# Kernel tuning notes

Hardware: AMD Instinct MI355X
Metric: run time of the kernel (lower is better)

## Reference

```python
import jax, jax.numpy as jnp
import numpy as np
from jax import lax

# dims (see shape_source)
B, T = 256, 32
DQ, K, S, CTX = 128, 8, 4, 16
D = 2 * DQ + 1            # state_flat = [q (DQ), p (DQ), extra (1)]
EVO, DT, DAMP, TAU = 8, 0.2, 0.1, 1.0
TOPK = 2
GAMMA = 10.0              # gamma_pred
EPS = 1e-8


def _router(q, ctx, Wq, Wc, b):
    # chart routing: softmax over K charts, temperature TAU
    return jax.nn.softmax((q @ Wq + ctx @ Wc + b) / TAU, axis=-1)


def _decode_topk(x, w, rw, rb):
    # x: [B,D], w: [B,K] chart weights -> [B,S] logits via top-k chart mixture
    logits_k = jnp.einsum('bd,kvd->bkv', x, rw) + rb          # [B,K,S]
    wv, idx = lax.top_k(w, TOPK)
    wn = wv / jnp.clip(wv.sum(-1, keepdims=True), EPS)
    wm = jnp.zeros_like(w).at[jnp.arange(w.shape[0])[:, None], idx].set(wn)
    return jnp.einsum('bkv,bk->bv', logits_k, wm)


def setup_inputs() -> dict:
    key = jax.random.key(0)
    ks = jax.random.split(key, 11)
    return {
        'inputs': jax.random.randint(ks[0], (B, T), 0, 2),
        'targets': jax.random.randint(ks[1], (B, T), 0, S),
        'task_ids': jax.random.randint(ks[2], (B, T), 0, 2),
        'initial_state_flat': jax.random.normal(ks[3], (B, D), jnp.float32),
        'bit_embed': jax.random.normal(ks[4], (2, DQ), jnp.float32),
        'task_u_embed': jax.random.normal(ks[5], (2, DQ), jnp.float32),
        'router_ctx_embed': jax.random.normal(ks[6], (2, CTX), jnp.float32),
        'readout_weight': 0.1 * jax.random.normal(ks[7], (K, S, D), jnp.float32),
        'readout_bias': jnp.zeros((K, S), jnp.float32),
        'router_Wq': 0.1 * jax.random.normal(ks[8], (DQ, K), jnp.float32),
        'router_Wc': 0.1 * jax.random.normal(ks[9], (CTX, K), jnp.float32),
        'router_b': jnp.zeros((K,), jnp.float32),
        'A': 0.02 * jax.random.normal(ks[10], (K, DQ, DQ), jnp.float32),
    }


def reference(inputs, targets, task_ids, initial_state_flat, bit_embed, task_u_embed,
              router_ctx_embed, readout_weight, readout_bias, router_Wq, router_Wc,
              router_b, A):
    Bn, Tn = inputs.shape
    rows = jnp.arange(Bn)
    targets_prev = jnp.concatenate([jnp.zeros_like(targets[:, :1]), targets[:, :-1]], axis=1)

    def step(carry, xs):
        state, tF, tacc, tce, usage, tsum, tcnt, scw, scnt = carry
        bit_t, target_t, prev_t, task_t = xs
        u = jnp.tanh(bit_embed[bit_t]) + jnp.tanh(task_u_embed[task_t])   # [B,DQ]
        ctx = jnp.tanh(router_ctx_embed[task_t])                          # [B,CTX]

        def evo(st, _):
            q, p, s = st[:, :DQ], st[:, DQ:2 * DQ], st[:, 2 * DQ:]
            w = _router(q, ctx, router_Wq, router_Wc, router_b)           # [B,K]
            # chart-weighted mixture-of-experts dynamics (semi-implicit, damped)
            force = jnp.einsum('bk,kij,bj->bi', w, A, jnp.tanh(q))
            p_new = (1.0 - DT * DAMP) * p + DT * (force + u)
            q_new = q + DT * jnp.tanh(p_new)
            return jnp.concatenate([q_new, p_new, s], axis=1), w

        state, ws = lax.scan(evo, state, None, length=EVO)
        chart_w = ws[-1]                                                  # router w from last evo step
        q = state[:, :DQ]
        chart_w_next = _router(q, ctx, router_Wq, router_Wc, router_b)
        logits = _decode_topk(state, chart_w_next, readout_weight, readout_bias)  # [B,S]
        logits2 = logits[:, :2]
        tgt2 = jnp.where(task_t == 0, target_t, 0)
        ce2 = -jax.nn.log_softmax(logits2, axis=-1)[rows, tgt2]
        ce4 = -jax.nn.log_softmax(logits, axis=-1)[rows, target_t]
        mask2 = (task_t == 0).astype(jnp.float32)
        pred_error = mask2 * ce2 + (1.0 - mask2) * ce4
        chart_state_loss = -jnp.log(jnp.clip(chart_w, EPS))[rows, prev_t]
        F_t = GAMMA * (pred_error + chart_state_loss)

        pred = jnp.where(task_t == 0, jnp.argmax(logits2, -1), jnp.argmax(logits, -1))
        correct = (pred == target_t).astype(jnp.float32)
        task_oh = jax.nn.one_hot(task_t, 2, dtype=jnp.float32)
        mask4 = (task_t == 1).astype(jnp.float32)[:, None]
        state_oh = jax.nn.one_hot(prev_t, S, dtype=jnp.float32)
        carry = (state,
                 tF + F_t.mean(),
                 tacc + correct.mean(),
                 tce + pred_error.mean(),
                 usage + chart_w.sum(0),
                 tsum + (correct[:, None] * task_oh).sum(0),
                 tcnt + task_oh.sum(0),
                 scw + (state_oh * mask4).T @ chart_w,
                 scnt + (state_oh * mask4).sum(0))
        return carry, None

    zf = jnp.zeros((), jnp.float32)
    init = (initial_state_flat, zf, zf, zf,
            jnp.zeros((K,), jnp.float32), jnp.zeros((2,), jnp.float32),
            jnp.zeros((2,), jnp.float32), jnp.zeros((S, K), jnp.float32),
            jnp.zeros((S,), jnp.float32))
    xs = (inputs.T, targets.T, targets_prev.T, task_ids.T)
    (state, tF, tacc, tce, usage, tsum, tcnt, scw, scnt), _ = lax.scan(step, init, xs)

    mean_F = tF / Tn
    mean_acc = tacc / Tn
    mean_ce = tce / Tn
    per_task_acc = tsum / (tcnt + EPS)
    dist = usage / (usage.sum() + EPS)
    chart_ent = -(dist * jnp.log(dist + EPS)).sum()
    joint = scw / (scw.sum() + EPS)
    p_s = joint.sum(1, keepdims=True)
    p_c = joint.sum(0, keepdims=True)
    mi = (joint * (jnp.log(joint + EPS) - jnp.log(p_s + EPS) - jnp.log(p_c + EPS))).sum()
    mi = jnp.where(scw.sum() > 0, jnp.clip(mi, 0.0), 0.0)
    return (mean_F, mean_acc, mean_ce, usage, chart_ent, per_task_acc, scw, scnt, mi)
```

## Files before the change

kernel.cpp:

```cpp
#include <hip/hip_runtime.h>
#include <hip/hip_fp16.h>

namespace {
constexpr int kT = 32, kDQ = 128, kK = 8, kS = 4, kCTX = 16, kD = 257, kEVO = 8;
constexpr float kDT = 0.2f, kDAMP = 0.1f, kGAMMA = 10.0f, kEPS = 1e-8f;

typedef _Float16 half8 __attribute__((ext_vector_type(8)));
typedef float f32x4 __attribute__((ext_vector_type(4)));
typedef unsigned u32x4 __attribute__((ext_vector_type(4)));

__device__ __forceinline__ unsigned packh2(float lo, float hi) {
  __half l = __float2half(lo), h = __float2half(hi);
  return (unsigned)__half_as_ushort(l) | ((unsigned)__half_as_ushort(h) << 16);
}
__device__ __forceinline__ float fast_tanh(float x) {
  float e = __expf(2.f * x);
  return 1.f - 2.f / (e + 1.f);
}
}

extern "C" __global__ void __launch_bounds__(512, 2)
seq_main(const int* __restrict__ inputs, const int* __restrict__ targets,
         const int* __restrict__ task_ids, const float* __restrict__ st0,
         const float* __restrict__ bit_emb, const float* __restrict__ task_u,
         const float* __restrict__ ctx_emb, const float* __restrict__ rw_g,
         const float* __restrict__ rb_g, const float* __restrict__ Wq_g,
         const float* __restrict__ Wc_g, const float* __restrict__ b_g,
         const float* __restrict__ A_g, float* __restrict__ ws) {
  const int tid = threadIdx.x, b = blockIdx.x;
  const int lane = tid & 63, w = tid >> 6;
  const int g = lane >> 4, c = lane & 15;
  const int g2 = lane >> 3, j = lane & 7;
  const int i_own = 16 * w + c;

  __shared__ __align__(16) float rw_l[kK * kS * kD];
  __shared__ __align__(16) float u4_l[4][kDQ];
  __shared__ __align__(16) float q_l[2][kDQ];
  __shared__ __align__(16) float p_l[kDQ];
  __shared__ __align__(16) unsigned tq_l[2][64];
  __shared__ __align__(16) float wq_ctx2[2][kK];
  __shared__ float chartw_l[kK];
  __shared__ float cwnext_l[kK];
  __shared__ float rb_l[kK * kS];
  __shared__ float lk_l[kK * kS];
  __shared__ float acc_l[64];
  __shared__ float s_l;

  for (int idx = tid; idx < kK * kS * kD; idx += 512) rw_l[idx] = rw_g[idx];
  if (tid < kK * kS) rb_l[tid] = rb_g[tid];
  if (tid == 0) s_l = st0[b * kD + 2 * kDQ];
  if (tid < 64) acc_l[tid] = 0.f;
  {
    int cb = tid >> 7, i = tid & 127;
    u4_l[cb][i] = tanhf(bit_emb[(cb & 1) * kDQ + i]) + tanhf(task_u[(cb >> 1) * kDQ + i]);
  }
  if (tid < 16) {
    int tk = tid >> 3, kk = tid & 7;
    float s = b_g[kk];
    #pragma unroll
    for (int cc = 0; cc < kCTX; cc++) s += tanhf(ctx_emb[tk * kCTX + cc]) * Wc_g[cc * kK + kk];
    wq_ctx2[tk][kk] = s;
  }

  const int kA = (c & 3) + 4 * ((c >> 3) & 1);
  const int ipar = (c >> 2) & 1;
  u32x4 afr[8][4];
  #pragma unroll
  for (int mt = 0; mt < 8; mt++) {
    const float* arow = A_g + ((size_t)kA * kDQ + (16 * w + 2 * mt + ipar)) * kDQ;
    #pragma unroll
    for (int ks = 0; ks < 4; ks++) {
      const float4* p4 = reinterpret_cast<const float4*>(arow + 32 * ks + 8 * g);
      float4 f0 = p4[0], f1 = p4[1];
      u32x4 v;
      v.x = packh2(f0.x, f0.y); v.y = packh2(f0.z, f0.w);
      v.z = packh2(f1.x, f1.y); v.w = packh2(f1.z, f1.w);
      afr[mt][ks] = v;
    }
  }
  float wqr[16];
  #pragma unroll
  for (int m = 0; m < 16; m++) wqr[m] = Wq_g[(16 * j + m) * kK + g2];

  float q = st0[b * kD + i_own];
  float p = st0[b * kD + kDQ + i_own];
  if (g == 0) {
    q_l[0][i_own] = q;
    float tv = fast_tanh(q);
    float to = __shfl_xor(tv, 1);
    if (!(c & 1)) tq_l[0][i_own >> 1] = packh2(tv, to);
  }
  __syncthreads();

  const float ctx0k = wq_ctx2[0][g2], ctx1k = wq_ctx2[1][g2];
  const int srl0 = 32 * (lane >> 5) + j;
  const int boff = b * kT;

  auto rdot = [&](const float* qb) -> float {
    const float4* q4 = reinterpret_cast<const float4*>(qb + 16 * j);
    float4 a0 = q4[0], a1 = q4[1], a2 = q4[2], a3 = q4[3];
    float part = a0.x * wqr[0] + a0.y * wqr[1] + a0.z * wqr[2] + a0.w * wqr[3]
               + a1.x * wqr[4] + a1.y * wqr[5] + a1.z * wqr[6] + a1.w * wqr[7]
               + a2.x * wqr[8] + a2.y * wqr[9] + a2.z * wqr[10] + a2.w * wqr[11]
               + a3.x * wqr[12] + a3.y * wqr[13] + a3.z * wqr[14] + a3.w * wqr[15];
    part += __shfl_xor(part, 1); part += __shfl_xor(part, 2); part += __shfl_xor(part, 4);
    return part;
  };
  auto rsmax = [&](float wlog, float ctxk) -> float {
    float lg = wlog + ctxk;
    float mx = lg;
    mx = fmaxf(mx, __shfl_xor(mx, 8));
    mx = fmaxf(mx, __shfl_xor(mx, 16));
    mx = fmaxf(mx, __shfl_xor(mx, 32));
    float ex = __expf(lg - mx);
    float sm = ex;
    sm += __shfl_xor(sm, 8); sm += __shfl_xor(sm, 16); sm += __shfl_xor(sm, 32);
    return ex / sm;
  };

  float ws0, ws1, ws2, ws3;
  {
    const int task0 = task_ids[boff];
    float wlog = rdot(q_l[0]);
    float wv = rsmax(wlog, task0 ? ctx1k : ctx0k);
    ws0 = __shfl(wv, srl0);      ws1 = __shfl(wv, srl0 + 8);
    ws2 = __shfl(wv, srl0 + 16); ws3 = __shfl(wv, srl0 + 24);
  }

  int sb = 0;
  for (int t = 0; t < kT; t++) {
    const int bit = inputs[boff + t];
    const int task = task_ids[boff + t];
    const int tasknx = (t < kT - 1) ? task_ids[boff + t + 1] : 0;
    const float u_own = u4_l[task * 2 + bit][i_own];

    for (int e = 0; e < kEVO; e++) {
      const u32x4* tq4 = reinterpret_cast<const u32x4*>(tq_l[sb]);
      f32x4 ac[8];
      #pragma unroll
      for (int mt = 0; mt < 8; mt++) ac[mt] = f32x4{0.f, 0.f, 0.f, 0.f};
      #pragma unroll
      for (int ks = 0; ks < 4; ks++) {
        half8 bf = __builtin_bit_cast(half8, tq4[4 * ks + g]);
        #pragma unroll
        for (int mt = 0; mt < 8; mt++)
          ac[mt] = __builtin_amdgcn_mfma_f32_16x16x32_f16(
              __builtin_bit_cast(half8, afr[mt][ks]), bf, ac[mt], 0, 0, 0);
      }
      float f0_, f1_, f2_, f3_, f4_, f5_, f6_, f7_;
      {
        float tmp[8];
        #pragma unroll
        for (int mt = 0; mt < 8; mt++) {
          float v = ws0 * ac[mt].x + ws1 * ac[mt].y + ws2 * ac[mt].z + ws3 * ac[mt].w;
          v += __shfl_xor(v, 32);
          tmp[mt] = v;
        }
        f0_ = tmp[0]; f1_ = tmp[1]; f2_ = tmp[2]; f3_ = tmp[3];
        f4_ = tmp[4]; f5_ = tmp[5]; f6_ = tmp[6]; f7_ = tmp[7];
      }
      const bool s0 = ((c >> 1) & 1), s1 = ((c >> 2) & 1), s2 = ((c >> 3) & 1);
      float a0 = s0 ? f1_ : f0_, a1 = s0 ? f3_ : f2_;
      float a2 = s0 ? f5_ : f4_, a3 = s0 ? f7_ : f6_;
      float b0 = s1 ? a1 : a0, b1 = s1 ? a3 : a2;
      float sel = s2 ? b1 : b0;
      float oth = __shfl_xor(sel, 16);
      float force = ((c ^ g) & 1) ? oth : sel;

      float pn = (1.f - kDT * kDAMP) * p + kDT * (force + u_own);
      q = q + kDT * fast_tanh(pn);
      p = pn;
      float tv = fast_tanh(q);
      if (g == 0) {
        float to = __shfl_xor(tv, 1);
        q_l[sb ^ 1][i_own] = q;
        if (!(c & 1)) tq_l[sb ^ 1][i_own >> 1] = packh2(tv, to);
        if (e == kEVO - 1) p_l[i_own] = p;
      }
      __syncthreads();

      float wlog = rdot(q_l[sb ^ 1]);
      float ctxn = (e < kEVO - 1) ? (task ? ctx1k : ctx0k) : (tasknx ? ctx1k : ctx0k);
      float wv = rsmax(wlog, ctxn);
      ws0 = __shfl(wv, srl0);      ws1 = __shfl(wv, srl0 + 8);
      ws2 = __shfl(wv, srl0 + 16); ws3 = __shfl(wv, srl0 + 24);
      if (e == kEVO - 2 && w == 0 && j == 0) chartw_l[g2] = wv;
      if (e == kEVO - 1) {
        float wvc = rsmax(wlog, task ? ctx1k : ctx0k);
        if (w == 0 && j == 0) cwnext_l[g2] = wvc;
      }
      sb ^= 1;
    }

    __syncthreads();
    {
      int pair = tid >> 4, ln = tid & 15;
      const float* rwrow = &rw_l[pair * kD];
      float sacc = 0.f;
      #pragma unroll
      for (int m = 0; m < 16; m++) {
        int d = ln + 16 * m;
        float sv = (m < 8) ? q_l[0][d] : p_l[d - kDQ];
        sacc += sv * rwrow[d];
      }
      if (ln == 0) sacc += s_l * rwrow[256];
      sacc += __shfl_xor(sacc, 1); sacc += __shfl_xor(sacc, 2);
      sacc += __shfl_xor(sacc, 4); sacc += __shfl_xor(sacc, 8);
      if (ln == 0) lk_l[pair] = sacc + rb_l[pair];
    }
    __syncthreads();
    if (tid == 0) {
      const int tgt = targets[boff + t];
      const int prv = (t == 0) ? 0 : targets[boff + t - 1];
      float cw[kK];
      #pragma unroll
      for (int kk = 0; kk < kK; kk++) cw[kk] = cwnext_l[kk];
      int i0 = 0; float v0 = cw[0];
      #pragma unroll
      for (int kk = 1; kk < kK; kk++) if (cw[kk] > v0) { v0 = cw[kk]; i0 = kk; }
      int i1 = (i0 == 0) ? 1 : 0; float v1 = cw[i1];
      #pragma unroll
      for (int kk = 0; kk < kK; kk++) if (kk != i0 && cw[kk] > v1) { v1 = cw[kk]; i1 = kk; }
      float wsum = fmaxf(v0 + v1, kEPS);
      float wn0 = v0 / wsum, wn1 = v1 / wsum;
      float lg4[4];
      #pragma unroll
      for (int v = 0; v < 4; v++) lg4[v] = wn0 * lk_l[i0 * 4 + v] + wn1 * lk_l[i1 * 4 + v];
      float m2 = fmaxf(lg4[0], lg4[1]);
      float lse2 = m2 + logf(expf(lg4[0] - m2) + expf(lg4[1] - m2));
      float m4 = fmaxf(fmaxf(lg4[0], lg4[1]), fmaxf(lg4[2], lg4[3]));
      float lse4 = m4 + logf(expf(lg4[0] - m4) + expf(lg4[1] - m4) + expf(lg4[2] - m4) + expf(lg4[3] - m4));
      int idx2 = (tgt < 1) ? tgt : 1;
      float p2 = (idx2 == 0) ? lg4[0] : lg4[1];
      float p4v = (tgt == 0) ? lg4[0] : ((tgt == 1) ? lg4[1] : ((tgt == 2) ? lg4[2] : lg4[3]));
      float ce2 = lse2 - p2, ce4 = lse4 - p4v;
      float pe = (task == 0) ? ce2 : ce4;
      int pred;
      if (task == 0) pred = (lg4[1] > lg4[0]) ? 1 : 0;
      else {
        pred = 0; float bv = lg4[0];
        if (lg4[1] > bv) { bv = lg4[1]; pred = 1; }
        if (lg4[2] > bv) { bv = lg4[2]; pred = 2; }
        if (lg4[3] > bv) { bv = lg4[3]; pred = 3; }
      }
      float corr = (pred == tgt) ? 1.f : 0.f;
      float csl = -logf(fmaxf(chartw_l[prv], kEPS));
      float Ft = kGAMMA * (pe + csl);
      acc_l[0] += Ft; acc_l[1] += corr; acc_l[2] += pe;
      #pragma unroll
      for (int kk = 0; kk < kK; kk++) acc_l[3 + kk] += chartw_l[kk];
      acc_l[11 + task] += corr; acc_l[13 + task] += 1.f;
      if (task == 1) {
        #pragma unroll
        for (int kk = 0; kk < kK; kk++) acc_l[15 + prv * kK + kk] += chartw_l[kk];
        acc_l[47 + prv] += 1.f;
      }
    }
    __syncthreads();
  }

  __syncthreads();
  if (tid < 64) ws[b * 64 + tid] = acc_l[tid];
}

extern "C" __global__ void seq_finalize(const float* __restrict__ ws, float* __restrict__ out) {
  const int tid = threadIdx.x;
  __shared__ float red[51];
  if (tid < 51) {
    float s = 0.f;
    for (int b = 0; b < 256; b++) s += ws[b * 64 + tid];
    red[tid] = s;
  }
  __syncthreads();
  if (tid == 0) {
    const float BT = 256.f * 32.f;
    out[0] = red[0] / BT;
    out[1] = red[1] / BT;
    out[2] = red[2] / BT;
    float us = 0.f;
    for (int k = 0; k < 8; k++) { out[3 + k] = red[3 + k]; us += red[3 + k]; }
    float ent = 0.f;
    for (int k = 0; k < 8; k++) {
      float dist = red[3 + k] / (us + kEPS);
      ent -= dist * logf(dist + kEPS);
    }
    out[11] = ent;
    out[12] = red[11] / (red[13] + kEPS);
    out[13] = red[12] / (red[14] + kEPS);
    float tot = 0.f;
    for (int jj = 0; jj < 32; jj++) { out[14 + jj] = red[15 + jj]; tot += red[15 + jj]; }
    for (int s2 = 0; s2 < 4; s2++) out[46 + s2] = red[47 + s2];
    float inv = 1.f / (tot + kEPS);
    float ps[4] = {0.f, 0.f, 0.f, 0.f};
    float pc[8] = {0.f, 0.f, 0.f, 0.f, 0.f, 0.f, 0.f, 0.f};
    for (int s2 = 0; s2 < 4; s2++)
      for (int k = 0; k < 8; k++) {
        float jv = red[15 + s2 * 8 + k] * inv;
        ps[s2] += jv; pc[k] += jv;
      }
    float mi = 0.f;
    for (int s2 = 0; s2 < 4; s2++)
      for (int k = 0; k < 8; k++) {
        float jv = red[15 + s2 * 8 + k] * inv;
        mi += jv * (logf(jv + kEPS) - logf(ps[s2] + kEPS) - logf(pc[k] + kEPS));
      }
    mi = (tot > 0.f) ? fmaxf(mi, 0.f) : 0.f;
    out[50] = mi;
  }
}

extern "C" void kernel_launch(void* const* d_in, const int* in_sizes, int n_in,
                              void* d_out, int out_size, void* d_ws, size_t ws_size,
                              hipStream_t stream) {
  (void)in_sizes; (void)n_in; (void)out_size; (void)ws_size;
  const int* inputs   = (const int*)d_in[0];
  const int* targets  = (const int*)d_in[1];
  const int* task_ids = (const int*)d_in[2];
  const float* st0      = (const float*)d_in[3];
  const float* bit_emb  = (const float*)d_in[4];
  const float* task_u   = (const float*)d_in[5];
  const float* ctx_emb  = (const float*)d_in[6];
  const float* rw       = (const float*)d_in[7];
  const float* rb       = (const float*)d_in[8];
  const float* Wq       = (const float*)d_in[9];
  const float* Wc       = (const float*)d_in[10];
  const float* bb       = (const float*)d_in[11];
  const float* A        = (const float*)d_in[12];
  float* ws  = (float*)d_ws;
  float* out = (float*)d_out;
  hipLaunchKernelGGL(seq_main, dim3(256), dim3(512), 0, stream,
                     inputs, targets, task_ids, st0, bit_emb, task_u, ctx_emb,
                     rw, rb, Wq, Wc, bb, A, ws);
  hipLaunchKernelGGL(seq_finalize, dim3(1), dim3(64), 0, stream, ws, out);
}
```

Before: 412.0 us.

## Batch 16 sequences per block so MFMA N dimension covers batch

```diff
diff --git a/kernel.cpp b/kernel.cpp
--- a/kernel.cpp
+++ b/kernel.cpp
@@ -2,16 +2,18 @@
 #include <hip/hip_fp16.h>
 
 namespace {
-constexpr int kT = 32, kDQ = 128, kK = 8, kS = 4, kCTX = 16, kD = 257, kEVO = 8;
+constexpr int kT = 32, kDQ = 128, kK = 8, kD = 257, kCTX = 16;
 constexpr float kDT = 0.2f, kDAMP = 0.1f, kGAMMA = 10.0f, kEPS = 1e-8f;
 
 typedef _Float16 half8 __attribute__((ext_vector_type(8)));
+typedef _Float16 h2 __attribute__((ext_vector_type(2)));
+typedef __fp16 fp16x2 __attribute__((ext_vector_type(2)));
 typedef float f32x4 __attribute__((ext_vector_type(4)));
 typedef unsigned u32x4 __attribute__((ext_vector_type(4)));
 
-__device__ __forceinline__ unsigned packh2(float lo, float hi) {
-  __half l = __float2half(lo), h = __float2half(hi);
-  return (unsigned)__half_as_ushort(l) | ((unsigned)__half_as_ushort(h) << 16);
+__device__ __forceinline__ unsigned pk16(float lo, float hi) {
+  fp16x2 r = __builtin_amdgcn_cvt_pkrtz(lo, hi);
+  return __builtin_bit_cast(unsigned, r);
 }
 __device__ __forceinline__ float fast_tanh(float x) {
   float e = __expf(2.f * x);
@@ -26,241 +28,339 @@
          const float* __restrict__ ctx_emb, const float* __restrict__ rw_g,
          const float* __restrict__ rb_g, const float* __restrict__ Wq_g,
          const float* __restrict__ Wc_g, const float* __restrict__ b_g,
-         const float* __restrict__ A_g, float* __restrict__ ws) {
-  const int tid = threadIdx.x, b = blockIdx.x;
-  const int lane = tid & 63, w = tid >> 6;
-  const int g = lane >> 4, c = lane & 15;
-  const int g2 = lane >> 3, j = lane & 7;
-  const int i_own = 16 * w + c;
-
-  __shared__ __align__(16) float rw_l[kK * kS * kD];
-  __shared__ __align__(16) float u4_l[4][kDQ];
-  __shared__ __align__(16) float q_l[2][kDQ];
-  __shared__ __align__(16) float p_l[kDQ];
-  __shared__ __align__(16) unsigned tq_l[2][64];
-  __shared__ __align__(16) float wq_ctx2[2][kK];
-  __shared__ float chartw_l[kK];
-  __shared__ float cwnext_l[kK];
-  __shared__ float rb_l[kK * kS];
-  __shared__ float lk_l[kK * kS];
-  __shared__ float acc_l[64];
-  __shared__ float s_l;
-
-  for (int idx = tid; idx < kK * kS * kD; idx += 512) rw_l[idx] = rw_g[idx];
-  if (tid < kK * kS) rb_l[tid] = rb_g[tid];
-  if (tid == 0) s_l = st0[b * kD + 2 * kDQ];
-  if (tid < 64) acc_l[tid] = 0.f;
+         const float* __restrict__ A_g, float* __restrict__ wsout) {
+  const int tid = threadIdx.x, blk = blockIdx.x;
+  const int l = tid & 63, w = tid >> 6;
+  const int b = l & 15, g4 = l >> 4;
+  const int i0 = 16 * w + 4 * g4;
+  const int dw0 = 8 * w + 2 * g4;
+
+  __shared__ __align__(16) unsigned q16_l[2][16][68];
+  __shared__ __align__(16) unsigned tq_l[2][16][68];
+  __shared__ __align__(16) unsigned p16_l[16][68];
+  __shared__ __align__(16) unsigned s16_l[16][16];
+  __shared__ __align__(16) unsigned rw16_l[32][148];
+  __shared__ __align__(16) float u4_l[4][128];
+  __shared__ __align__(16) float chartw_l[16][12];
+  __shared__ __align__(16) float cwnext_l[16][12];
+  __shared__ float rb_l[32];
+  __shared__ int sel_l[32][16];
+  __shared__ int task_l[32][16];
+  __shared__ int tgt_l[32][16];
+  __shared__ float lk_l[16][36];
+  __shared__ float scw_l[32];
+  __shared__ float scnt_l[4];
+
+  if (tid < 32) scw_l[tid] = 0.f;
+  if (tid < 4) scnt_l[tid] = 0.f;
+  if (tid < 32) rb_l[tid] = rb_g[tid];
+  {
+    int t = tid >> 4, bb = tid & 15;
+    int gb = blk * 16 + bb;
+    int bit = inputs[gb * kT + t];
+    int task = task_ids[gb * kT + t];
+    sel_l[t][bb] = task * 2 + bit;
+    task_l[t][bb] = task;
+    tgt_l[t][bb] = targets[gb * kT + t];
+  }
   {
     int cb = tid >> 7, i = tid & 127;
     u4_l[cb][i] = tanhf(bit_emb[(cb & 1) * kDQ + i]) + tanhf(task_u[(cb >> 1) * kDQ + i]);
   }
-  if (tid < 16) {
-    int tk = tid >> 3, kk = tid & 7;
-    float s = b_g[kk];
-    #pragma unroll
-    for (int cc = 0; cc < kCTX; cc++) s += tanhf(ctx_emb[tk * kCTX + cc]) * Wc_g[cc * kK + kk];
-    wq_ctx2[tk][kk] = s;
-  }
-
-  const int kA = (c & 3) + 4 * ((c >> 3) & 1);
-  const int ipar = (c >> 2) & 1;
+  for (int idx = tid; idx < 32 * 148; idx += 512) {
+    int pr = idx / 148, dw = idx - pr * 148;
+    int d0 = 2 * dw;
+    float lo = (d0 < 257) ? rw_g[pr * 257 + d0] : 0.f;
+    float hi = (d0 + 1 < 257) ? rw_g[pr * 257 + d0 + 1] : 0.f;
+    rw16_l[pr][dw] = pk16(lo, hi);
+  }
+  if (tid < 256) {
+    int bb = tid >> 4, dw = tid & 15;
+    s16_l[bb][dw] = (dw == 0) ? pk16(st0[(blk * 16 + bb) * kD + 256], 0.f) : 0u;
+  }
+
   u32x4 afr[8][4];
   #pragma unroll
-  for (int mt = 0; mt < 8; mt++) {
-    const float* arow = A_g + ((size_t)kA * kDQ + (16 * w + 2 * mt + ipar)) * kDQ;
-    #pragma unroll
-    for (int ks = 0; ks < 4; ks++) {
-      const float4* p4 = reinterpret_cast<const float4*>(arow + 32 * ks + 8 * g);
-      float4 f0 = p4[0], f1 = p4[1];
+  for (int k = 0; k < 8; ++k) {
+    #pragma unroll
+    for (int ks = 0; ks < 4; ++ks) {
+      const float* ap = A_g + ((size_t)(k * kDQ + 16 * w + b)) * kDQ + 32 * ks + 8 * g4;
+      float4 fa = *(const float4*)ap;
+      float4 fb = *(const float4*)(ap + 4);
       u32x4 v;
-      v.x = packh2(f0.x, f0.y); v.y = packh2(f0.z, f0.w);
-      v.z = packh2(f1.x, f1.y); v.w = packh2(f1.z, f1.w);
-      afr[mt][ks] = v;
-    }
-  }
-  float wqr[16];
+      v.x = pk16(fa.x, fa.y); v.y = pk16(fa.z, fa.w);
+      v.z = pk16(fb.x, fb.y); v.w = pk16(fb.z, fb.w);
+      afr[k][ks] = v;
+    }
+  }
+  u32x4 wqf[4];
   #pragma unroll
-  for (int m = 0; m < 16; m++) wqr[m] = Wq_g[(16 * j + m) * kK + g2];
-
-  float q = st0[b * kD + i_own];
-  float p = st0[b * kD + kDQ + i_own];
-  if (g == 0) {
-    q_l[0][i_own] = q;
-    float tv = fast_tanh(q);
-    float to = __shfl_xor(tv, 1);
-    if (!(c & 1)) tq_l[0][i_own >> 1] = packh2(tv, to);
-  }
+  for (int ks = 0; ks < 4; ++ks) {
+    float e_[8];
+    #pragma unroll
+    for (int e = 0; e < 8; ++e)
+      e_[e] = (b < 8) ? Wq_g[(32 * ks + 8 * g4 + e) * kK + b] : 0.f;
+    u32x4 v;
+    v.x = pk16(e_[0], e_[1]); v.y = pk16(e_[2], e_[3]);
+    v.z = pk16(e_[4], e_[5]); v.w = pk16(e_[6], e_[7]);
+    wqf[ks] = v;
+  }
+  float ctx0[4], ctx1[4];
+  #pragma unroll
+  for (int r = 0; r < 4; ++r) {
+    int k = 4 * g4 + r;
+    float s0v = 0.f, s1v = 0.f;
+    if (k < 8) {
+      s0v = b_g[k]; s1v = b_g[k];
+      #pragma unroll
+      for (int c = 0; c < kCTX; ++c) {
+        float wc = Wc_g[c * kK + k];
+        s0v += tanhf(ctx_emb[c]) * wc;
+        s1v += tanhf(ctx_emb[kCTX + c]) * wc;
+      }
+    }
+    ctx0[r] = s0v; ctx1[r] = s1v;
+  }
+  float q[4], p[4];
+  {
+    const int gb = blk * 16 + b;
+    #pragma unroll
+    for (int r = 0; r < 4; ++r) {
+      q[r] = st0[gb * kD + i0 + r];
+      p[r] = st0[gb * kD + kDQ + i0 + r];
+    }
+  }
+  q16_l[0][b][dw0] = pk16(q[0], q[1]);
+  q16_l[0][b][dw0 + 1] = pk16(q[2], q[3]);
+  tq_l[0][b][dw0] = pk16(fast_tanh(q[0]), fast_tanh(q[1]));
+  tq_l[0][b][dw0 + 1] = pk16(fast_tanh(q[2]), fast_tanh(q[3]));
+
+  float aF = 0.f, aC = 0.f, aPE = 0.f;
+  float aU[8] = {0.f, 0.f, 0.f, 0.f, 0.f, 0.f, 0.f, 0.f};
+  float aTS0 = 0.f, aTS1 = 0.f, aTC0 = 0.f, aTC1 = 0.f;
+
+  float w8[8];
+
+  auto runR = [&](int step) {
+    const int nb_ = (step + 1) & 1;
+    int snx = step + 1; if (snx > 255) snx = 255;
+    const int tn = task_l[snx >> 3][b];
+    f32x4 wacc = {0.f, 0.f, 0.f, 0.f};
+    #pragma unroll
+    for (int ks = 0; ks < 4; ++ks) {
+      u32x4 bq = *(const u32x4*)&q16_l[nb_][b][ks * 16 + 4 * g4];
+      wacc = __builtin_amdgcn_mfma_f32_16x16x32_f16(
+          __builtin_bit_cast(half8, wqf[ks]), __builtin_bit_cast(half8, bq), wacc, 0, 0, 0);
+    }
+    float lg[4];
+    #pragma unroll
+    for (int r = 0; r < 4; ++r) lg[r] = wacc[r] + (tn ? ctx1[r] : ctx0[r]);
+    float m = fmaxf(fmaxf(lg[0], lg[1]), fmaxf(lg[2], lg[3]));
+    m = fmaxf(m, __shfl_xor(m, 16));
+    float e0 = __expf(lg[0] - m), e1 = __expf(lg[1] - m);
+    float e2 = __expf(lg[2] - m), e3 = __expf(lg[3] - m);
+    float s = e0 + e1 + e2 + e3;
+    s += __shfl_xor(s, 16);
+    float inv = 1.f / s;
+    float w0 = e0 * inv, w1 = e1 * inv, w2 = e2 * inv, w3 = e3 * inv;
+    if (step >= 0 && (step & 7) == 6 && w == 3 && g4 < 2) {
+      f32x4 cv = {w0, w1, w2, w3};
+      *(f32x4*)&chartw_l[b][4 * g4] = cv;
+    }
+    if (step >= 0 && (step & 7) == 7) {
+      const int tc = task_l[step >> 3][b];
+      float lh[4];
+      #pragma unroll
+      for (int r = 0; r < 4; ++r) lh[r] = wacc[r] + (tc ? ctx1[r] : ctx0[r]);
+      float m2 = fmaxf(fmaxf(lh[0], lh[1]), fmaxf(lh[2], lh[3]));
+      m2 = fmaxf(m2, __shfl_xor(m2, 16));
+      float f0 = __expf(lh[0] - m2), f1 = __expf(lh[1] - m2);
+      float f2 = __expf(lh[2] - m2), f3 = __expf(lh[3] - m2);
+      float s2 = f0 + f1 + f2 + f3;
+      s2 += __shfl_xor(s2, 16);
+      float i2 = 1.f / s2;
+      if (w == 3 && g4 < 2) {
+        f32x4 cv = {f0 * i2, f1 * i2, f2 * i2, f3 * i2};
+        *(f32x4*)&cwnext_l[b][4 * g4] = cv;
+      }
+    }
+    int pk01 = (int)pk16(w0, w1), pk23 = (int)pk16(w2, w3);
+    int alo = 4 * b, ahi = 4 * (16 + b);
+    int r01l = __builtin_amdgcn_ds_bpermute(alo, pk01);
+    int r23l = __builtin_amdgcn_ds_bpermute(alo, pk23);
+    int r01h = __builtin_amdgcn_ds_bpermute(ahi, pk01);
+    int r23h = __builtin_amdgcn_ds_bpermute(ahi, pk23);
+    h2 v;
+    v = __builtin_bit_cast(h2, r01l); w8[0] = (float)v.x; w8[1] = (float)v.y;
+    v = __builtin_bit_cast(h2, r23l); w8[2] = (float)v.x; w8[3] = (float)v.y;
+    v = __builtin_bit_cast(h2, r01h); w8[4] = (float)v.x; w8[5] = (float)v.y;
+    v = __builtin_bit_cast(h2, r23h); w8[6] = (float)v.x; w8[7] = (float)v.y;
+  };
+
+  auto runDecode = [&]() {
+    const int pair = 16 * w + b;
+    f32x4 dacc = {0.f, 0.f, 0.f, 0.f};
+    #pragma unroll
+    for (int ks = 0; ks < 4; ++ks) {
+      u32x4 aq = *(const u32x4*)&q16_l[0][b][ks * 16 + 4 * g4];
+      u32x4 bq = *(const u32x4*)&rw16_l[pair][ks * 16 + 4 * g4];
+      dacc = __builtin_amdgcn_mfma_f32_16x16x32_f16(
+          __builtin_bit_cast(half8, aq), __builtin_bit_cast(half8, bq), dacc, 0, 0, 0);
+    }
+    #pragma unroll
+    for (int ks = 4; ks < 8; ++ks) {
+      u32x4 aq = *(const u32x4*)&p16_l[b][(ks - 4) * 16 + 4 * g4];
+      u32x4 bq = *(const u32x4*)&rw16_l[pair][ks * 16 + 4 * g4];
+      dacc = __builtin_amdgcn_mfma_f32_16x16x32_f16(
+          __builtin_bit_cast(half8, aq), __builtin_bit_cast(half8, bq), dacc, 0, 0, 0);
+    }
+    {
+      u32x4 aq = *(const u32x4*)&s16_l[b][4 * g4];
+      u32x4 bq = *(const u32x4*)&rw16_l[pair][128 + 4 * g4];
+      dacc = __builtin_amdgcn_mfma_f32_16x16x32_f16(
+          __builtin_bit_cast(half8, aq), __builtin_bit_cast(half8, bq), dacc, 0, 0, 0);
+    }
+    #pragma unroll
+    for (int r = 0; r < 4; ++r) lk_l[4 * g4 + r][pair] = dacc[r];
+  };
+
+  auto runTail = [&](int t) {
+    if (l >= 16) return;
+    const int bb = l;
+    const int tgt = tgt_l[t][bb];
+    const int task = task_l[t][bb];
+    const int prv = (t == 0) ? 0 : tgt_l[t - 1][bb];
+    f32x4 ca = *(const f32x4*)&cwnext_l[bb][0];
+    f32x4 cbv = *(const f32x4*)&cwnext_l[bb][4];
+    float cw[8] = {ca.x, ca.y, ca.z, ca.w, cbv.x, cbv.y, cbv.z, cbv.w};
+    f32x4 ha = *(const f32x4*)&chartw_l[bb][0];
+    f32x4 hb = *(const f32x4*)&chartw_l[bb][4];
+    float ch[8] = {ha.x, ha.y, ha.z, ha.w, hb.x, hb.y, hb.z, hb.w};
+    int i0_ = 0; float v0 = cw[0];
+    #pragma unroll
+    for (int kk = 1; kk < 8; ++kk) if (cw[kk] > v0) { v0 = cw[kk]; i0_ = kk; }
+    int i1_ = (i0_ == 0) ? 1 : 0;
+    float v1 = (i0_ == 0) ? cw[1] : cw[0];
+    #pragma unroll
+    for (int kk = 0; kk < 8; ++kk) if (kk != i0_ && cw[kk] > v1) { v1 = cw[kk]; i1_ = kk; }
+    float wsum = fmaxf(v0 + v1, kEPS);
+    float wn0 = v0 / wsum, wn1 = v1 / wsum;
+    float lg4[4];
+    #pragma unroll
+    for (int v = 0; v < 4; ++v)
+      lg4[v] = wn0 * (lk_l[bb][i0_ * 4 + v] + rb_l[i0_ * 4 + v]) +
+               wn1 * (lk_l[bb][i1_ * 4 + v] + rb_l[i1_ * 4 + v]);
+    float m2 = fmaxf(lg4[0], lg4[1]);
+    float lse2 = m2 + logf(expf(lg4[0] - m2) + expf(lg4[1] - m2));
+    float m4 = fmaxf(fmaxf(lg4[0], lg4[1]), fmaxf(lg4[2], lg4[3]));
+    float lse4 = m4 + logf(expf(lg4[0] - m4) + expf(lg4[1] - m4) +
+                           expf(lg4[2] - m4) + expf(lg4[3] - m4));
+    int idx2 = (tgt < 1) ? tgt : 1;
+    float p2 = (idx2 == 0) ? lg4[0] : lg4[1];
+    float p4v = (tgt == 0) ? lg4[0] : ((tgt == 1) ? lg4[1] : ((tgt == 2) ? lg4[2] : lg4[3]));
+    float ce2 = lse2 - p2, ce4 = lse4 - p4v;
+    float pe = (task == 0) ? ce2 : ce4;
+    int pred;
+    if (task == 0) pred = (lg4[1] > lg4[0]) ? 1 : 0;
+    else {
+      pred = 0; float bv = lg4[0];
+      if (lg4[1] > bv) { bv = lg4[1]; pred = 1; }
+      if (lg4[2] > bv) { bv = lg4[2]; pred = 2; }
+      if (lg4[3] > bv) { bv = lg4[3]; pred = 3; }
+    }
+    float corr = (pred == tgt) ? 1.f : 0.f;
+    float chprv = chartw_l[bb][prv];
+    float csl = -logf(fmaxf(chprv, kEPS));
+    float Ft = kGAMMA * (pe + csl);
+    aF += Ft; aC += corr; aPE += pe;
+    #pragma unroll
+    for (int kk = 0; kk < 8; ++kk) aU[kk] += ch[kk];
+    if (task == 0) { aTS0 += corr; aTC0 += 1.f; }
+    else {
+      aTS1 += corr; aTC1 += 1.f;
+      #pragma unroll
+      for (int kk = 0; kk < 8; ++kk) atomicAdd(&scw_l[prv * 8 + kk], ch[kk]);
+      atomicAdd(&scnt_l[prv], 1.f);
+    }
+  };
+
   __syncthreads();
-
-  const float ctx0k = wq_ctx2[0][g2], ctx1k = wq_ctx2[1][g2];
-  const int srl0 = 32 * (lane >> 5) + j;
-  const int boff = b * kT;
-
-  auto rdot = [&](const float* qb) -> float {
-    const float4* q4 = reinterpret_cast<const float4*>(qb + 16 * j);
-    float4 a0 = q4[0], a1 = q4[1], a2 = q4[2], a3 = q4[3];
-    float part = a0.x * wqr[0] + a0.y * wqr[1] + a0.z * wqr[2] + a0.w * wqr[3]
-               + a1.x * wqr[4] + a1.y * wqr[5] + a1.z * wqr[6] + a1.w * wqr[7]
-               + a2.x * wqr[8] + a2.y * wqr[9] + a2.z * wqr[10] + a2.w * wqr[11]
-               + a3.x * wqr[12] + a3.y * wqr[13] + a3.z * wqr[14] + a3.w * wqr[15];
-    part += __shfl_xor(part, 1); part += __shfl_xor(part, 2); part += __shfl_xor(part, 4);
-    return part;
-  };
-  auto rsmax = [&](float wlog, float ctxk) -> float {
-    float lg = wlog + ctxk;
-    float mx = lg;
-    mx = fmaxf(mx, __shfl_xor(mx, 8));
-    mx = fmaxf(mx, __shfl_xor(mx, 16));
-    mx = fmaxf(mx, __shfl_xor(mx, 32));
-    float ex = __expf(lg - mx);
-    float sm = ex;
-    sm += __shfl_xor(sm, 8); sm += __shfl_xor(sm, 16); sm += __shfl_xor(sm, 32);
-    return ex / sm;
-  };
-
-  float ws0, ws1, ws2, ws3;
-  {
-    const int task0 = task_ids[boff];
-    float wlog = rdot(q_l[0]);
-    float wv = rsmax(wlog, task0 ? ctx1k : ctx0k);
-    ws0 = __shfl(wv, srl0);      ws1 = __shfl(wv, srl0 + 8);
-    ws2 = __shfl(wv, srl0 + 16); ws3 = __shfl(wv, srl0 + 24);
-  }
-
-  int sb = 0;
-  for (int t = 0; t < kT; t++) {
-    const int bit = inputs[boff + t];
-    const int task = task_ids[boff + t];
-    const int tasknx = (t < kT - 1) ? task_ids[boff + t + 1] : 0;
-    const float u_own = u4_l[task * 2 + bit][i_own];
-
-    for (int e = 0; e < kEVO; e++) {
-      const u32x4* tq4 = reinterpret_cast<const u32x4*>(tq_l[sb]);
-      f32x4 ac[8];
-      #pragma unroll
-      for (int mt = 0; mt < 8; mt++) ac[mt] = f32x4{0.f, 0.f, 0.f, 0.f};
-      #pragma unroll
-      for (int ks = 0; ks < 4; ks++) {
-        half8 bf = __builtin_bit_cast(half8, tq4[4 * ks + g]);
-        #pragma unroll
-        for (int mt = 0; mt < 8; mt++)
-          ac[mt] = __builtin_amdgcn_mfma_f32_16x16x32_f16(
-              __builtin_bit_cast(half8, afr[mt][ks]), bf, ac[mt], 0, 0, 0);
-      }
-      float f0_, f1_, f2_, f3_, f4_, f5_, f6_, f7_;
-      {
-        float tmp[8];
-        #pragma unroll
-        for (int mt = 0; mt < 8; mt++) {
-          float v = ws0 * ac[mt].x + ws1 * ac[mt].y + ws2 * ac[mt].z + ws3 * ac[mt].w;
-          v += __shfl_xor(v, 32);
-          tmp[mt] = v;
-        }
-        f0_ = tmp[0]; f1_ = tmp[1]; f2_ = tmp[2]; f3_ = tmp[3];
-        f4_ = tmp[4]; f5_ = tmp[5]; f6_ = tmp[6]; f7_ = tmp[7];
-      }
-      const bool s0 = ((c >> 1) & 1), s1 = ((c >> 2) & 1), s2 = ((c >> 3) & 1);
-      float a0 = s0 ? f1_ : f0_, a1 = s0 ? f3_ : f2_;
-      float a2 = s0 ? f5_ : f4_, a3 = s0 ? f7_ : f6_;
-      float b0 = s1 ? a1 : a0, b1 = s1 ? a3 : a2;
-      float sel = s2 ? b1 : b0;
-      float oth = __shfl_xor(sel, 16);
-      float force = ((c ^ g) & 1) ? oth : sel;
-
-      float pn = (1.f - kDT * kDAMP) * p + kDT * (force + u_own);
-      q = q + kDT * fast_tanh(pn);
-      p = pn;
-      float tv = fast_tanh(q);
-      if (g == 0) {
-        float to = __shfl_xor(tv, 1);
-        q_l[sb ^ 1][i_own] = q;
-        if (!(c & 1)) tq_l[sb ^ 1][i_own >> 1] = packh2(tv, to);
-        if (e == kEVO - 1) p_l[i_own] = p;
-      }
-      __syncthreads();
-
-      float wlog = rdot(q_l[sb ^ 1]);
-      float ctxn = (e < kEVO - 1) ? (task ? ctx1k : ctx0k) : (tasknx ? ctx1k : ctx0k);
-      float wv = rsmax(wlog, ctxn);
-      ws0 = __shfl(wv, srl0);      ws1 = __shfl(wv, srl0 + 8);
-      ws2 = __shfl(wv, srl0 + 16); ws3 = __shfl(wv, srl0 + 24);
-      if (e == kEVO - 2 && w == 0 && j == 0) chartw_l[g2] = wv;
-      if (e == kEVO - 1) {
-        float wvc = rsmax(wlog, task ? ctx1k : ctx0k);
-        if (w == 0 && j == 0) cwnext_l[g2] = wvc;
-      }
-      sb ^= 1;
-    }
-
+  runR(-1);
+
+  float u_own[4] = {0.f, 0.f, 0.f, 0.f};
+  #pragma unroll 1
+  for (int step = 0; step < 256; ++step) {
+    const int cb_ = step & 1, nb_ = cb_ ^ 1;
+    const int e = step & 7, t = step >> 3;
+    if (e == 0) {
+      int sel = sel_l[t][b];
+      f32x4 uu = *(const f32x4*)&u4_l[sel][i0];
+      u_own[0] = uu.x; u_own[1] = uu.y; u_own[2] = uu.z; u_own[3] = uu.w;
+    }
+    f32x4 ac[8];
+    #pragma unroll
+    for (int k = 0; k < 8; ++k) ac[k] = f32x4{0.f, 0.f, 0.f, 0.f};
+    #pragma unroll
+    for (int ks = 0; ks < 4; ++ks) {
+      u32x4 bq = *(const u32x4*)&tq_l[cb_][b][ks * 16 + 4 * g4];
+      half8 bf = __builtin_bit_cast(half8, bq);
+      #pragma unroll
+      for (int k = 0; k < 8; ++k)
+        ac[k] = __builtin_amdgcn_mfma_f32_16x16x32_f16(
+            __builtin_bit_cast(half8, afr[k][ks]), bf, ac[k], 0, 0, 0);
+    }
+    #pragma unroll
+    for (int r = 0; r < 4; ++r) {
+      float f = w8[0] * ac[0][r] + w8[1] * ac[1][r] + w8[2] * ac[2][r] + w8[3] * ac[3][r] +
+                w8[4] * ac[4][r] + w8[5] * ac[5][r] + w8[6] * ac[6][r] + w8[7] * ac[7][r];
+      float pn = (1.f - kDT * kDAMP) * p[r] + kDT * (f + u_own[r]);
+      q[r] += kDT * fast_tanh(pn);
+      p[r] = pn;
+    }
+    q16_l[nb_][b][dw0] = pk16(q[0], q[1]);
+    q16_l[nb_][b][dw0 + 1] = pk16(q[2], q[3]);
+    tq_l[nb_][b][dw0] = pk16(fast_tanh(q[0]), fast_tanh(q[1]));
+    tq_l[nb_][b][dw0 + 1] = pk16(fast_tanh(q[2]), fast_tanh(q[3]));
+    if (e == 7) {
+      p16_l[b][dw0] = pk16(p[0], p[1]);
+      p16_l[b][dw0 + 1] = pk16(p[2], p[3]);
+    }
+    if (e == 0 && step != 0 && w < 2) runDecode();
+    if (e == 1 && step > 8 && w == 2) runTail(t - 1);
     __syncthreads();
-    {
-      int pair = tid >> 4, ln = tid & 15;
-      const float* rwrow = &rw_l[pair * kD];
-      float sacc = 0.f;
-      #pragma unroll
-      for (int m = 0; m < 16; m++) {
-        int d = ln + 16 * m;
-        float sv = (m < 8) ? q_l[0][d] : p_l[d - kDQ];
-        sacc += sv * rwrow[d];
-      }
-      if (ln == 0) sacc += s_l * rwrow[256];
-      sacc += __shfl_xor(sacc, 1); sacc += __shfl_xor(sacc, 2);
-      sacc += __shfl_xor(sacc, 4); sacc += __shfl_xor(sacc, 8);
-      if (ln == 0) lk_l[pair] = sacc + rb_l[pair];
-    }
-    __syncthreads();
-    if (tid == 0) {
-      const int tgt = targets[boff + t];
-      const int prv = (t == 0) ? 0 : targets[boff + t - 1];
-      float cw[kK];
-      #pragma unroll
-      for (int kk = 0; kk < kK; kk++) cw[kk] = cwnext_l[kk];
-      int i0 = 0; float v0 = cw[0];
-      #pragma unroll
-      for (int kk = 1; kk < kK; kk++) if (cw[kk] > v0) { v0 = cw[kk]; i0 = kk; }
-      int i1 = (i0 == 0) ? 1 : 0; float v1 = cw[i1];
-      #pragma unroll
-      for (int kk = 0; kk < kK; kk++) if (kk != i0 && cw[kk] > v1) { v1 = cw[kk]; i1 = kk; }
-      float wsum = fmaxf(v0 + v1, kEPS);
-      float wn0 = v0 / wsum, wn1 = v1 / wsum;
-      float lg4[4];
-      #pragma unroll
-      for (int v = 0; v < 4; v++) lg4[v] = wn0 * lk_l[i0 * 4 + v] + wn1 * lk_l[i1 * 4 + v];
-      float m2 = fmaxf(lg4[0], lg4[1]);
-      float lse2 = m2 + logf(expf(lg4[0] - m2) + expf(lg4[1] - m2));
-      float m4 = fmaxf(fmaxf(lg4[0], lg4[1]), fmaxf(lg4[2], lg4[3]));
-      float lse4 = m4 + logf(expf(lg4[0] - m4) + expf(lg4[1] - m4) + expf(lg4[2] - m4) + expf(lg4[3] - m4));
-      int idx2 = (tgt < 1) ? tgt : 1;
-      float p2 = (idx2 == 0) ? lg4[0] : lg4[1];
-      float p4v = (tgt == 0) ? lg4[0] : ((tgt == 1) ? lg4[1] : ((tgt == 2) ? lg4[2] : lg4[3]));
-      float ce2 = lse2 - p2, ce4 = lse4 - p4v;
-      float pe = (task == 0) ? ce2 : ce4;
-      int pred;
-      if (task == 0) pred = (lg4[1] > lg4[0]) ? 1 : 0;
-      else {
-        pred = 0; float bv = lg4[0];
-        if (lg4[1] > bv) { bv = lg4[1]; pred = 1; }
-        if (lg4[2] > bv) { bv = lg4[2]; pred = 2; }
-        if (lg4[3] > bv) { bv = lg4[3]; pred = 3; }
-      }
-      float corr = (pred == tgt) ? 1.f : 0.f;
-      float csl = -logf(fmaxf(chartw_l[prv], kEPS));
-      float Ft = kGAMMA * (pe + csl);
-      acc_l[0] += Ft; acc_l[1] += corr; acc_l[2] += pe;
-      #pragma unroll
-      for (int kk = 0; kk < kK; kk++) acc_l[3 + kk] += chartw_l[kk];
-      acc_l[11 + task] += corr; acc_l[13 + task] += 1.f;
-      if (task == 1) {
-        #pragma unroll
-        for (int kk = 0; kk < kK; kk++) acc_l[15 + prv * kK + kk] += chartw_l[kk];
-        acc_l[47 + prv] += 1.f;
-      }
-    }
-    __syncthreads();
+    runR(step);
   }
 
   __syncthreads();
-  if (tid < 64) ws[b * 64 + tid] = acc_l[tid];
+  if (w < 2) runDecode();
+  __syncthreads();
+  if (w == 2) runTail(31);
+  __syncthreads();
+
+  if (w == 2) {
+    float vF = aF, vC = aC, vPE = aPE;
+    float vTS0 = aTS0, vTS1 = aTS1, vTC0 = aTC0, vTC1 = aTC1;
+    float vU[8];
+    #pragma unroll
+    for (int kk = 0; kk < 8; ++kk) vU[kk] = aU[kk];
+    #pragma unroll
+    for (int d = 1; d < 16; d <<= 1) {
+      vF += __shfl_xor(vF, d); vC += __shfl_xor(vC, d); vPE += __shfl_xor(vPE, d);
+      vTS0 += __shfl_xor(vTS0, d); vTS1 += __shfl_xor(vTS1, d);
+      vTC0 += __shfl_xor(vTC0, d); vTC1 += __shfl_xor(vTC1, d);
+      #pragma unroll
+      for (int kk = 0; kk < 8; ++kk) vU[kk] += __shfl_xor(vU[kk], d);
+    }
+    if (l == 0) {
+      float* wo = wsout + blk * 64;
+      wo[0] = vF; wo[1] = vC; wo[2] = vPE;
+      #pragma unroll
+      for (int kk = 0; kk < 8; ++kk) wo[3 + kk] = vU[kk];
+      wo[11] = vTS0; wo[12] = vTS1; wo[13] = vTC0; wo[14] = vTC1;
+    }
+    if (l < 32) wsout[blk * 64 + 15 + l] = scw_l[l];
+    if (l < 4) wsout[blk * 64 + 47 + l] = scnt_l[l];
+  }
 }
 
 extern "C" __global__ void seq_finalize(const float* __restrict__ ws, float* __restrict__ out) {
@@ -268,7 +368,7 @@
   __shared__ float red[51];
   if (tid < 51) {
     float s = 0.f;
-    for (int b = 0; b < 256; b++) s += ws[b * 64 + tid];
+    for (int blk = 0; blk < 16; ++blk) s += ws[blk * 64 + tid];
     red[tid] = s;
   }
   __syncthreads();
@@ -288,7 +388,7 @@
     out[12] = red[11] / (red[13] + kEPS);
     out[13] = red[12] / (red[14] + kEPS);
     float tot = 0.f;
-    for (int jj = 0; jj < 32; jj++) { out[14 + jj] = red[15 + jj]; tot += red[15 + jj]; }
+    for (int j = 0; j < 32; j++) { out[14 + j] = red[15 + j]; tot += red[15 + j]; }
     for (int s2 = 0; s2 < 4; s2++) out[46 + s2] = red[47 + s2];
     float inv = 1.f / (tot + kEPS);
     float ps[4] = {0.f, 0.f, 0.f, 0.f};
@@ -328,7 +428,7 @@
   const float* A        = (const float*)d_in[12];
   float* ws  = (float*)d_ws;
   float* out = (float*)d_out;
-  hipLaunchKernelGGL(seq_main, dim3(256), dim3(512), 0, stream,
+  hipLaunchKernelGGL(seq_main, dim3(16), dim3(512), 0, stream,
                      inputs, targets, task_ids, st0, bit_emb, task_u, ctx_emb,
                      rw, rb, Wq, Wc, bb, A, ws);
   hipLaunchKernelGGL(seq_finalize, dim3(1), dim3(64), 0, stream, ws, out);
```

Result: slower. 497.6 us (+20.8%).
